# Kernel tuning notes

Hardware: AMD Instinct MI355X
Metric: run time of the kernel (lower is better)

Reference implementation:

```python
import jax, jax.numpy as jnp
import numpy as np

B, S, D = 4, 2048, 512
E, K = 8, 2
MH = 4 * D      # resmlp mlp hidden
EH = 2 * D      # expert hidden
EPS = 1e-5


def setup_inputs() -> dict:
    key = jax.random.key(0)
    ks = jax.random.split(key, 16)
    s = 0.02
    return {
        "x": jax.random.normal(ks[0], (B, S, D), dtype=jnp.float32),
        "ln1_g": jnp.ones((D,), jnp.float32), "ln1_b": jnp.zeros((D,), jnp.float32),
        "w1": jax.random.normal(ks[1], (D, MH), jnp.float32) * s,
        "b1": jnp.zeros((MH,), jnp.float32),
        "w2": jax.random.normal(ks[2], (MH, D), jnp.float32) * s,
        "b2": jnp.zeros((D,), jnp.float32),
        "ln2_g": jnp.ones((D,), jnp.float32), "ln2_b": jnp.zeros((D,), jnp.float32),
        "wr": jax.random.normal(ks[3], (E, D), jnp.float32) * s,
        "ew1": jax.random.normal(ks[4], (E, D, EH), jnp.float32) * s,
        "eb1": jnp.zeros((E, EH), jnp.float32),
        "ew2": jax.random.normal(ks[5], (E, EH, D), jnp.float32) * s,
        "eb2": jnp.zeros((E, D), jnp.float32),
        "lnf_g": jnp.ones((D,), jnp.float32), "lnf_b": jnp.zeros((D,), jnp.float32),
    }


def _ln(z, g, b):
    m = z.mean(-1, keepdims=True)
    v = ((z - m) ** 2).mean(-1, keepdims=True)
    return (z - m) * jax.lax.rsqrt(v + EPS) * g + b


def reference(x, ln1_g, ln1_b, w1, b1, w2, b2, ln2_g, ln2_b,
              wr, ew1, eb1, ew2, eb2, lnf_g, lnf_b):
    # ---- ResidualMLPBlock (eval mode: dropout is identity) ----
    h = _ln(x, ln1_g, ln1_b)
    h = jax.nn.gelu(h @ w1 + b1, approximate=False) @ w2 + b2
    x = x + h
    x = _ln(x, ln2_g, ln2_b) + x
    # ---- MoE (eval: no jitter noise, aux_loss = 0) ----
    xf = x.reshape(-1, D)              # [N, D], N = B*S
    n = xf.shape[0]
    probs = jax.nn.softmax(xf @ wr.T, axis=-1)          # [N, E]
    topv, topi = jax.lax.top_k(probs, K)                # [N, K]
    topv = topv / topv.sum(-1, keepdims=True)
    # dense per-token gate per expert: sum over k of renormalized prob where idx==j
    gates = jnp.zeros((n, E), xf.dtype).at[jnp.arange(n)[:, None], topi].add(topv)
    # per-expert MLP over all tokens (masked scatter-combine via gates)
    he = jax.nn.gelu(jnp.einsum("nd,edh->enh", xf, ew1) + eb1[:, None, :],
                     approximate=False)                 # [E, N, 2D]
    ye = jnp.einsum("enh,ehd->end", he, ew2) + eb2[:, None, :]  # [E, N, D]
    out = jnp.einsum("ne,end->nd", gates, ye).reshape(B, S, D)
    # ---- final LayerNorm ----
    out = _ln(out, lnf_g, lnf_b)
    aux_loss = jnp.zeros((), x.dtype)  # eval mode
    return out, aux_loss
```

## Files before the change

### kernel.cpp

```cpp
#include <hip/hip_runtime.h>

#define NTOK 8192
#define DIM  512
#define MHID 2048
#define EHID 1024
#define NEXP 8
#define RBLK 64

using half_t = _Float16;
typedef _Float16 f16x8 __attribute__((ext_vector_type(8)));
typedef float    f32x16 __attribute__((ext_vector_type(16)));

#define MFMA32(a, b, c) __builtin_amdgcn_mfma_f32_32x32x16_f16((a), (b), (c), 0, 0, 0)

typedef const __attribute__((address_space(1))) void* gas_ptr;
typedef __attribute__((address_space(3))) void*       las_ptr;
__device__ __forceinline__ void gl16(const void* g, void* l) {
    __builtin_amdgcn_global_load_lds((gas_ptr)g, (las_ptr)l, 16, 0, 0);
}

__device__ __forceinline__ float gelu_exact(float v) {
    return 0.5f * v * (1.0f + erff(v * 0.70710678118654752f));
}

__device__ __forceinline__ float block_sum4(float v, float* red, int tid) {
#pragma unroll
    for (int off = 32; off; off >>= 1) v += __shfl_down(v, off);
    if ((tid & 63) == 0) red[tid >> 6] = v;
    __syncthreads();
    float r = red[0] + red[1] + red[2] + red[3];
    __syncthreads();
    return r;
}

__global__ __launch_bounds__(256) void ln1_split_kernel(
    const float* __restrict__ x, const float* __restrict__ g, const float* __restrict__ b,
    half_t* __restrict__ xh, half_t* __restrict__ xl)
{
    const int row = blockIdx.x, tid = threadIdx.x;
    __shared__ float red[4];
    const size_t base = (size_t)row * DIM;
    float2 v = reinterpret_cast<const float2*>(x + base)[tid];
    float mean = block_sum4(v.x + v.y, red, tid) * (1.0f / DIM);
    float d0 = v.x - mean, d1 = v.y - mean;
    float var = block_sum4(d0 * d0 + d1 * d1, red, tid) * (1.0f / DIM);
    float rstd = rsqrtf(var + 1e-5f);
    int d = tid * 2;
    float y0 = d0 * rstd * g[d]     + b[d];
    float y1 = d1 * rstd * g[d + 1] + b[d + 1];
    half_t h0 = (half_t)y0, h1 = (half_t)y1;
    xh[base + d] = h0;  xh[base + d + 1] = h1;
    xl[base + d]     = (half_t)(y0 - (float)h0);
    xl[base + d + 1] = (half_t)(y1 - (float)h1);
}

__global__ __launch_bounds__(256) void resid_ln2_kernel(
    const float* __restrict__ x, float* __restrict__ p0, const float* __restrict__ p1,
    const float* __restrict__ b2,
    const float* __restrict__ g, const float* __restrict__ b,
    half_t* __restrict__ x3h)
{
    const int row = blockIdx.x, tid = threadIdx.x;
    __shared__ float red[4];
    const size_t base = (size_t)row * DIM;
    float2 xv = reinterpret_cast<const float2*>(x + base)[tid];
    float2 h0 = reinterpret_cast<float2*>(p0 + base)[tid];
    float2 h1 = reinterpret_cast<const float2*>(p1 + base)[tid];
    float2 bb = reinterpret_cast<const float2*>(b2)[tid];
    float z0 = xv.x + h0.x + h1.x + bb.x, z1 = xv.y + h0.y + h1.y + bb.y;
    float mean = block_sum4(z0 + z1, red, tid) * (1.0f / DIM);
    float d0 = z0 - mean, d1 = z1 - mean;
    float var = block_sum4(d0 * d0 + d1 * d1, red, tid) * (1.0f / DIM);
    float rstd = rsqrtf(var + 1e-5f);
    int d = tid * 2;
    float y0 = d0 * rstd * g[d]     + b[d]     + z0;
    float y1 = d1 * rstd * g[d + 1] + b[d + 1] + z1;
    float2 o; o.x = y0; o.y = y1;
    reinterpret_cast<float2*>(p0 + base)[tid] = o;
    x3h[base + d]     = (half_t)y0;
    x3h[base + d + 1] = (half_t)y1;
}

__global__ void transpose_split_kernel(const float* __restrict__ in,
                                       half_t* __restrict__ oh, half_t* __restrict__ ol,
                                       int R, int C)
{
    __shared__ float t[32][33];
    const size_t mo = (size_t)blockIdx.z * (size_t)R * (size_t)C;
    const int c0 = blockIdx.x * 32, r0 = blockIdx.y * 32;
    const int tx = threadIdx.x, ty = threadIdx.y;
    for (int i = ty; i < 32; i += 8) t[i][tx] = in[mo + (size_t)(r0 + i) * C + c0 + tx];
    __syncthreads();
    for (int i = ty; i < 32; i += 8) {
        float v = t[tx][i];
        size_t o = mo + (size_t)(c0 + i) * R + r0 + tx;
        half_t h = (half_t)v;
        oh[o] = h;
        if (ol) ol[o] = (half_t)(v - (float)h);
    }
}

template <int EPI>
__global__ __launch_bounds__(256) void gemm3_kernel(
    const half_t* __restrict__ A0, const half_t* __restrict__ A1,
    const half_t* __restrict__ B0, const half_t* __restrict__ B1,
    const float* __restrict__ bias,
    float* __restrict__ Cf0, float* __restrict__ Cf1,
    half_t* __restrict__ Ch, half_t* __restrict__ Cl,
    int Nc, int K, int Ktile)
{
    __shared__ __align__(16) half_t As0[128 * 32];
    __shared__ __align__(16) half_t As1[128 * 32];
    __shared__ __align__(16) half_t Bs0[128 * 32];
    __shared__ __align__(16) half_t Bs1[128 * 32];
    const int m0 = blockIdx.x * 128, n0 = blockIdx.y * 128;
    const int kbeg = blockIdx.z * Ktile;
    float* Cf = blockIdx.z ? Cf1 : Cf0;
    const int tid = threadIdx.x;
    const int lane = tid & 63, wid = tid >> 6;
    const int wr = wid >> 1, wc = wid & 1;

    const int c0 = tid, c1 = tid + 256;
    const int r0 = c0 >> 2, s0 = (c0 & 3) ^ ((r0 >> 1) & 3);
    const int r1 = c1 >> 2, s1 = (c1 & 3) ^ ((r1 >> 1) & 3);
    const size_t aoff0 = (size_t)(m0 + r0) * K + kbeg + s0 * 8;
    const size_t aoff1 = (size_t)(m0 + r1) * K + kbeg + s1 * 8;
    const size_t boff0 = (size_t)(n0 + r0) * K + kbeg + s0 * 8;
    const size_t boff1 = (size_t)(n0 + r1) * K + kbeg + s1 * 8;

    const int l31 = lane & 31, l5 = lane >> 5;
    int oa[2][2], ob[2][2];
#pragma unroll
    for (int i = 0; i < 2; i++)
#pragma unroll
        for (int kh = 0; kh < 2; kh++) {
            int ra = wr * 64 + i * 32 + l31;
            oa[i][kh] = ra * 32 + (((l5 + kh * 2) ^ ((ra >> 1) & 3)) << 3);
            int rb = wc * 64 + i * 32 + l31;
            ob[i][kh] = rb * 32 + (((l5 + kh * 2) ^ ((rb >> 1) & 3)) << 3);
        }

    f32x16 acc[2][2];
#pragma unroll
    for (int i = 0; i < 2; i++)
#pragma unroll
        for (int j = 0; j < 2; j++)
#pragma unroll
            for (int q = 0; q < 16; q++) acc[i][j][q] = 0.f;

#pragma unroll 1
    for (int k0 = 0; k0 < Ktile; k0 += 32) {
        __syncthreads();
        gl16(A0 + aoff0 + k0, As0 + c0 * 8);
        gl16(A0 + aoff1 + k0, As0 + c1 * 8);
        gl16(A1 + aoff0 + k0, As1 + c0 * 8);
        gl16(A1 + aoff1 + k0, As1 + c1 * 8);
        gl16(B0 + boff0 + k0, Bs0 + c0 * 8);
        gl16(B0 + boff1 + k0, Bs0 + c1 * 8);
        gl16(B1 + boff0 + k0, Bs1 + c0 * 8);
        gl16(B1 + boff1 + k0, Bs1 + c1 * 8);
        __syncthreads();
#pragma unroll
        for (int kh = 0; kh < 2; kh++) {
            f16x8 ah0 = *(const f16x8*)(As0 + oa[0][kh]);
            f16x8 ah1 = *(const f16x8*)(As0 + oa[1][kh]);
            f16x8 al0 = *(const f16x8*)(As1 + oa[0][kh]);
            f16x8 al1 = *(const f16x8*)(As1 + oa[1][kh]);
            f16x8 bh0 = *(const f16x8*)(Bs0 + ob[0][kh]);
            f16x8 bh1 = *(const f16x8*)(Bs0 + ob[1][kh]);
            f16x8 bl0 = *(const f16x8*)(Bs1 + ob[0][kh]);
            f16x8 bl1 = *(const f16x8*)(Bs1 + ob[1][kh]);
            acc[0][0] = MFMA32(ah0, bh0, acc[0][0]);
            acc[0][0] = MFMA32(al0, bh0, acc[0][0]);
            acc[0][0] = MFMA32(ah0, bl0, acc[0][0]);
            acc[0][1] = MFMA32(ah0, bh1, acc[0][1]);
            acc[0][1] = MFMA32(al0, bh1, acc[0][1]);
            acc[0][1] = MFMA32(ah0, bl1, acc[0][1]);
            acc[1][0] = MFMA32(ah1, bh0, acc[1][0]);
            acc[1][0] = MFMA32(al1, bh0, acc[1][0]);
            acc[1][0] = MFMA32(ah1, bl0, acc[1][0]);
            acc[1][1] = MFMA32(ah1, bh1, acc[1][1]);
            acc[1][1] = MFMA32(al1, bh1, acc[1][1]);
            acc[1][1] = MFMA32(ah1, bl1, acc[1][1]);
        }
    }

    const int er = 4 * l5;
#pragma unroll
    for (int i = 0; i < 2; i++)
#pragma unroll
        for (int j = 0; j < 2; j++) {
            int cc = n0 + wc * 64 + j * 32 + l31;
            float bv = (EPI == 1) ? bias[cc] : 0.f;
#pragma unroll
            for (int reg = 0; reg < 16; reg++) {
                int rr = m0 + wr * 64 + i * 32 + er + 8 * (reg >> 2) + (reg & 3);
                float v = acc[i][j][reg] + bv;
                size_t o = (size_t)rr * Nc + cc;
                if (EPI == 1) {
                    float ge = gelu_exact(v);
                    half_t h = (half_t)ge;
                    Ch[o] = h;
                    Cl[o] = (half_t)(ge - (float)h);
                } else {
                    Cf[o] = v;
                }
            }
        }
}

__global__ __launch_bounds__(256) void router_kernel(
    const float* __restrict__ x3, const float* __restrict__ wrm,
    int* __restrict__ cnt, int* __restrict__ aid, float* __restrict__ gate)
{
    __shared__ float wl[NEXP][DIM];
    __shared__ int   texp[RBLK * 2];
    __shared__ float tgate[RBLK * 2];
    __shared__ int   lslot[RBLK * 2];
    __shared__ int   lcnt[NEXP], lbase[NEXP];
    const int tid = threadIdx.x;
    for (int i = tid; i < NEXP * DIM / 4; i += 256)
        reinterpret_cast<float4*>(&wl[0][0])[i] = reinterpret_cast<const float4*>(wrm)[i];
    if (tid < NEXP) lcnt[tid] = 0;
    __syncthreads();
    const int w = tid >> 6, lane = tid & 63;
#pragma unroll 1
    for (int t = 0; t < RBLK / 4; ++t) {
        const int lt = w * (RBLK / 4) + t;
        const int token = blockIdx.x * RBLK + lt;
        const float* xr = x3 + (size_t)token * DIM;
        float a[NEXP];
#pragma unroll
        for (int e = 0; e < NEXP; e++) a[e] = 0.f;
#pragma unroll
        for (int d0 = 0; d0 < DIM; d0 += 64) {
            float xv = xr[d0 + lane];
#pragma unroll
            for (int e = 0; e < NEXP; e++) a[e] += xv * wl[e][d0 + lane];
        }
#pragma unroll
        for (int e = 0; e < NEXP; e++)
#pragma unroll
            for (int off = 32; off; off >>= 1) a[e] += __shfl_xor(a[e], off);
        if (lane == 0) {
            int i1 = 0; float v1 = a[0];
#pragma unroll
            for (int e = 1; e < NEXP; e++) if (a[e] > v1) { v1 = a[e]; i1 = e; }
            int i2 = -1; float v2 = -3.4e38f;
#pragma unroll
            for (int e = 0; e < NEXP; e++) if (e != i1 && a[e] > v2) { v2 = a[e]; i2 = e; }
            float e2 = expf(v2 - v1);
            float g1 = 1.0f / (1.0f + e2);
            texp[lt * 2]      = i1; tgate[lt * 2]      = g1;
            texp[lt * 2 + 1]  = i2; tgate[lt * 2 + 1]  = 1.0f - g1;
        }
    }
    __syncthreads();
    if (tid < RBLK * 2) lslot[tid] = atomicAdd(&lcnt[texp[tid]], 1);
    __syncthreads();
    if (tid < NEXP) lbase[tid] = atomicAdd(&cnt[tid * 32], lcnt[tid]);
    __syncthreads();
    if (tid < RBLK * 2) {
        const int e = texp[tid];
        const int asg = blockIdx.x * (RBLK * 2) + tid;
        aid[e * NTOK + lbase[e] + lslot[tid]] = asg;
        gate[asg] = tgate[tid];
    }
}

__global__ __launch_bounds__(256) void egemm1_kernel(
    const half_t* __restrict__ X,
    const half_t* __restrict__ W,
    const float* __restrict__ eb1,
    const int* __restrict__ cnt, const int* __restrict__ aid,
    half_t* __restrict__ He)
{
    const int bid = blockIdx.x;
    const int e = bid >> 9, rem = bid & 511;
    const int mt = rem >> 3, nt = rem & 7;
    const int ne = cnt[e * 32];
    if (mt * 128 >= ne) return;
    __shared__ __align__(16) half_t As[128 * 32];
    __shared__ __align__(16) half_t Bs[128 * 32];
    __shared__ int rowmap[128];
    const int tid = threadIdx.x;
    if (tid < 128) {
        int slot = mt * 128 + tid;
        rowmap[tid] = (slot < ne) ? aid[e * NTOK + slot] : -1;
    }
    __syncthreads();
    const int lane = tid & 63, wid = tid >> 6;
    const int wr = wid >> 1, wc = wid & 1;
    const int c0 = tid, c1 = tid + 256;
    const int r0 = c0 >> 2, s0 = (c0 & 3) ^ ((r0 >> 1) & 3);
    const int r1 = c1 >> 2, s1 = (c1 & 3) ^ ((r1 >> 1) & 3);
    const int a0r = rowmap[r0], a1r = rowmap[r1];
    const half_t* pa0 = X + (size_t)(a0r >= 0 ? (a0r >> 1) : 0) * DIM + s0 * 8;
    const half_t* pa1 = X + (size_t)(a1r >= 0 ? (a1r >> 1) : 0) * DIM + s1 * 8;
    const half_t* pb0 = W + (size_t)e * EHID * DIM + (size_t)(nt * 128 + r0) * DIM + s0 * 8;
    const half_t* pb1 = W + (size_t)e * EHID * DIM + (size_t)(nt * 128 + r1) * DIM + s1 * 8;

    const int l31 = lane & 31, l5 = lane >> 5;
    int oa[2][2], ob[2][2];
#pragma unroll
    for (int i = 0; i < 2; i++)
#pragma unroll
        for (int kh = 0; kh < 2; kh++) {
            int ra = wr * 64 + i * 32 + l31;
            oa[i][kh] = ra * 32 + (((l5 + kh * 2) ^ ((ra >> 1) & 3)) << 3);
            int rb = wc * 64 + i * 32 + l31;
            ob[i][kh] = rb * 32 + (((l5 + kh * 2) ^ ((rb >> 1) & 3)) << 3);
        }
    f32x16 acc[2][2];
#pragma unroll
    for (int i = 0; i < 2; i++)
#pragma unroll
        for (int j = 0; j < 2; j++)
#pragma unroll
            for (int q = 0; q < 16; q++) acc[i][j][q] = 0.f;

#pragma unroll 1
    for (int k0 = 0; k0 < DIM; k0 += 32) {
        __syncthreads();
        gl16(pa0 + k0, As + c0 * 8);
        gl16(pa1 + k0, As + c1 * 8);
        gl16(pb0 + k0, Bs + c0 * 8);
        gl16(pb1 + k0, Bs + c1 * 8);
        __syncthreads();
#pragma unroll
        for (int kh = 0; kh < 2; kh++) {
            f16x8 a0 = *(const f16x8*)(As + oa[0][kh]);
            f16x8 a1 = *(const f16x8*)(As + oa[1][kh]);
            f16x8 b0 = *(const f16x8*)(Bs + ob[0][kh]);
            f16x8 b1 = *(const f16x8*)(Bs + ob[1][kh]);
            acc[0][0] = MFMA32(a0, b0, acc[0][0]);
            acc[0][1] = MFMA32(a0, b1, acc[0][1]);
            acc[1][0] = MFMA32(a1, b0, acc[1][0]);
            acc[1][1] = MFMA32(a1, b1, acc[1][1]);
        }
    }
    const int er = 4 * l5;
#pragma unroll
    for (int i = 0; i < 2; i++)
#pragma unroll
        for (int reg = 0; reg < 16; reg++) {
            int rloc = wr * 64 + i * 32 + er + 8 * (reg >> 2) + (reg & 3);
            int a = rowmap[rloc];
            if (a >= 0) {
#pragma unroll
                for (int j = 0; j < 2; j++) {
                    int cc = nt * 128 + wc * 64 + j * 32 + l31;
                    float v = acc[i][j][reg] + eb1[e * EHID + cc];
                    He[(size_t)a * EHID + cc] = (half_t)gelu_exact(v);
                }
            }
        }
}

__global__ __launch_bounds__(256) void egemm2_kernel(
    const half_t* __restrict__ Hin,
    const half_t* __restrict__ W,
    const float* __restrict__ eb2,
    const int* __restrict__ cnt, const int* __restrict__ aid,
    const float* __restrict__ gate,
    float* __restrict__ Ye)
{
    const int bid = blockIdx.x;
    const int e = bid >> 8, rem = bid & 255;
    const int mt = rem >> 2, nt = rem & 3;
    const int ne = cnt[e * 32];
    if (mt * 128 >= ne) return;
    __shared__ __align__(16) half_t As[128 * 32];
    __shared__ __align__(16) half_t Bs[128 * 32];
    __shared__ int rowmap[128];
    const int tid = threadIdx.x;
    if (tid < 128) {
        int slot = mt * 128 + tid;
        rowmap[tid] = (slot < ne) ? aid[e * NTOK + slot] : -1;
    }
    __syncthreads();
    const int lane = tid & 63, wid = tid >> 6;
    const int wr = wid >> 1, wc = wid & 1;
    const int c0 = tid, c1 = tid + 256;
    const int r0 = c0 >> 2, s0 = (c0 & 3) ^ ((r0 >> 1) & 3);
    const int r1 = c1 >> 2, s1 = (c1 & 3) ^ ((r1 >> 1) & 3);
    const int a0r = rowmap[r0], a1r = rowmap[r1];
    const half_t* pa0 = Hin + (size_t)(a0r >= 0 ? a0r : 0) * EHID + s0 * 8;
    const half_t* pa1 = Hin + (size_t)(a1r >= 0 ? a1r : 0) * EHID + s1 * 8;
    const half_t* pb0 = W + (size_t)e * DIM * EHID + (size_t)(nt * 128 + r0) * EHID + s0 * 8;
    const half_t* pb1 = W + (size_t)e * DIM * EHID + (size_t)(nt * 128 + r1) * EHID + s1 * 8;

    const int l31 = lane & 31, l5 = lane >> 5;
    int oa[2][2], ob[2][2];
#pragma unroll
    for (int i = 0; i < 2; i++)
#pragma unroll
        for (int kh = 0; kh < 2; kh++) {
            int ra = wr * 64 + i * 32 + l31;
            oa[i][kh] = ra * 32 + (((l5 + kh * 2) ^ ((ra >> 1) & 3)) << 3);
            int rb = wc * 64 + i * 32 + l31;
            ob[i][kh] = rb * 32 + (((l5 + kh * 2) ^ ((rb >> 1) & 3)) << 3);
        }
    f32x16 acc[2][2];
#pragma unroll
    for (int i = 0; i < 2; i++)
#pragma unroll
        for (int j = 0; j < 2; j++)
#pragma unroll
            for (int q = 0; q < 16; q++) acc[i][j][q] = 0.f;

#pragma unroll 1
    for (int k0 = 0; k0 < EHID; k0 += 32) {
        __syncthreads();
        gl16(pa0 + k0, As + c0 * 8);
        gl16(pa1 + k0, As + c1 * 8);
        gl16(pb0 + k0, Bs + c0 * 8);
        gl16(pb1 + k0, Bs + c1 * 8);
        __syncthreads();
#pragma unroll
        for (int kh = 0; kh < 2; kh++) {
            f16x8 a0 = *(const f16x8*)(As + oa[0][kh]);
            f16x8 a1 = *(const f16x8*)(As + oa[1][kh]);
            f16x8 b0 = *(const f16x8*)(Bs + ob[0][kh]);
            f16x8 b1 = *(const f16x8*)(Bs + ob[1][kh]);
            acc[0][0] = MFMA32(a0, b0, acc[0][0]);
            acc[0][1] = MFMA32(a0, b1, acc[0][1]);
            acc[1][0] = MFMA32(a1, b0, acc[1][0]);
            acc[1][1] = MFMA32(a1, b1, acc[1][1]);
        }
    }
    const int er = 4 * l5;
#pragma unroll
    for (int i = 0; i < 2; i++)
#pragma unroll
        for (int reg = 0; reg < 16; reg++) {
            int rloc = wr * 64 + i * 32 + er + 8 * (reg >> 2) + (reg & 3);
            int a = rowmap[rloc];
            if (a >= 0) {
                float gv = gate[a];
#pragma unroll
                for (int j = 0; j < 2; j++) {
                    int cc = nt * 128 + wc * 64 + j * 32 + l31;
                    float v = (acc[i][j][reg] + eb2[e * DIM + cc]) * gv;
                    Ye[(size_t)a * DIM + cc] = v;
                }
            }
        }
}

__global__ __launch_bounds__(256) void combine_lnf_kernel(
    const float* __restrict__ Ye, const float* __restrict__ g, const float* __restrict__ b,
    float* __restrict__ out)
{
    const int t = blockIdx.x, tid = threadIdx.x;
    __shared__ float red[4];
    float2 y0 = reinterpret_cast<const float2*>(Ye + (size_t)(2 * t) * DIM)[tid];
    float2 y1 = reinterpret_cast<const float2*>(Ye + (size_t)(2 * t + 1) * DIM)[tid];
    float z0 = y0.x + y1.x, z1 = y0.y + y1.y;
    float mean = block_sum4(z0 + z1, red, tid) * (1.0f / DIM);
    float d0 = z0 - mean, d1 = z1 - mean;
    float var = block_sum4(d0 * d0 + d1 * d1, red, tid) * (1.0f / DIM);
    float rstd = rsqrtf(var + 1e-5f);
    int d = tid * 2;
    out[(size_t)t * DIM + d]     = d0 * rstd * g[d]     + b[d];
    out[(size_t)t * DIM + d + 1] = d1 * rstd * g[d + 1] + b[d + 1];
    if (t == 0 && tid == 0) out[(size_t)NTOK * DIM] = 0.f;
}

__global__ void zero_cnt_kernel(int* cnt) {
    cnt[threadIdx.x] = 0;
}

extern "C" void kernel_launch(void* const* d_in, const int* in_sizes, int n_in,
                              void* d_out, int out_size, void* d_ws, size_t ws_size,
                              hipStream_t stream)
{
    (void)in_sizes; (void)n_in; (void)out_size; (void)ws_size;
    const float* x    = (const float*)d_in[0];
    const float* ln1g = (const float*)d_in[1];
    const float* ln1b = (const float*)d_in[2];
    const float* w1   = (const float*)d_in[3];
    const float* b1   = (const float*)d_in[4];
    const float* w2   = (const float*)d_in[5];
    const float* b2   = (const float*)d_in[6];
    const float* ln2g = (const float*)d_in[7];
    const float* ln2b = (const float*)d_in[8];
    const float* wrm  = (const float*)d_in[9];
    const float* ew1  = (const float*)d_in[10];
    const float* eb1  = (const float*)d_in[11];
    const float* ew2  = (const float*)d_in[12];
    const float* eb2  = (const float*)d_in[13];
    const float* lnfg = (const float*)d_in[14];
    const float* lnfb = (const float*)d_in[15];
    float* out = (float*)d_out;

    char* w = (char*)d_ws;
    size_t off = 0;
    auto take = [&](size_t bytes) {
        char* p = w + off;
        off += bytes;
        off = (off + 255) & ~(size_t)255;
        return p;
    };
    half_t* xh_h  = (half_t*)take((size_t)NTOK * DIM * 2);
    half_t* xh_l  = (half_t*)take((size_t)NTOK * DIM * 2);
    half_t* w1t_h = (half_t*)take((size_t)DIM * MHID * 2);
    half_t* w1t_l = (half_t*)take((size_t)DIM * MHID * 2);
    half_t* w2t_h = (half_t*)take((size_t)MHID * DIM * 2);
    half_t* w2t_l = (half_t*)take((size_t)MHID * DIM * 2);
    char*   big   = take((size_t)NTOK * MHID * 2 * 2);
    half_t* a1h   = (half_t*)big;
    half_t* a1l   = (half_t*)(big + (size_t)NTOK * MHID * 2);
    half_t* heh   = (half_t*)big;
    float*  yef   = (float*)(big + (size_t)NTOK * MHID * 2);
    float*  x3f   = (float*)take((size_t)NTOK * DIM * 4);
    half_t* x3h   = (half_t*)take((size_t)NTOK * DIM * 2);
    half_t* ew1t  = (half_t*)take((size_t)NEXP * DIM * EHID * 2);
    half_t* ew2t  = (half_t*)take((size_t)NEXP * EHID * DIM * 2);
    int*    cnt   = (int*)take(1024);
    int*    aid   = (int*)take((size_t)NEXP * NTOK * 4);
    float*  gate  = (float*)take((size_t)NTOK * 2 * 4);

    float* p0 = x3f;
    float* p1 = (float*)xh_h;

    zero_cnt_kernel<<<1, 256, 0, stream>>>(cnt);
    ln1_split_kernel<<<NTOK, 256, 0, stream>>>(x, ln1g, ln1b, xh_h, xh_l);
    transpose_split_kernel<<<dim3(MHID / 32, DIM / 32, 1), dim3(32, 8), 0, stream>>>(w1, w1t_h, w1t_l, DIM, MHID);
    transpose_split_kernel<<<dim3(DIM / 32, MHID / 32, 1), dim3(32, 8), 0, stream>>>(w2, w2t_h, w2t_l, MHID, DIM);
    transpose_split_kernel<<<dim3(EHID / 32, DIM / 32, NEXP), dim3(32, 8), 0, stream>>>(ew1, ew1t, (half_t*)0, DIM, EHID);
    transpose_split_kernel<<<dim3(DIM / 32, EHID / 32, NEXP), dim3(32, 8), 0, stream>>>(ew2, ew2t, (half_t*)0, EHID, DIM);
    gemm3_kernel<1><<<dim3(NTOK / 128, MHID / 128, 1), 256, 0, stream>>>(
        xh_h, xh_l, w1t_h, w1t_l, b1, (float*)0, (float*)0, a1h, a1l, MHID, DIM, DIM);
    gemm3_kernel<0><<<dim3(NTOK / 128, DIM / 128, 2), 256, 0, stream>>>(
        a1h, a1l, w2t_h, w2t_l, (const float*)0, p0, p1, (half_t*)0, (half_t*)0, DIM, MHID, MHID / 2);
    resid_ln2_kernel<<<NTOK, 256, 0, stream>>>(x, p0, p1, b2, ln2g, ln2b, x3h);
    router_kernel<<<NTOK / RBLK, 256, 0, stream>>>(x3f, wrm, cnt, aid, gate);
    egemm1_kernel<<<NEXP * (NTOK / 128) * (EHID / 128), 256, 0, stream>>>(x3h, ew1t, eb1, cnt, aid, heh);
    egemm2_kernel<<<NEXP * (NTOK / 128) * (DIM / 128), 256, 0, stream>>>(heh, ew2t, eb2, cnt, aid, gate, yef);
    combine_lnf_kernel<<<NTOK, 256, 0, stream>>>(yef, lnfg, lnfb, out);
}
```

Baseline: 324.4 us.

## Double-buffer LDS tiles in dense and expert GEMM kernels

Converts the shared-memory A/B tiles of gemm3, egemm1 and egemm2 to two buffers each. The next K-slice is now issued with global_load_lds before computing on the current one, so the MFMA work can overlap the global-to-LDS traffic instead of stalling at every slice. This doubles LDS use per block (64KB for the split-f16 gemm3), which may lower occupancy. The loop steps two slices at a time and assumes the K extent is a multiple of 64.

```diff
diff --git a/kernel.cpp b/kernel.cpp
--- a/kernel.cpp
+++ b/kernel.cpp
@@ -109,10 +109,10 @@
     half_t* __restrict__ Ch, half_t* __restrict__ Cl,
     int Nc, int K, int Ktile)
 {
-    __shared__ __align__(16) half_t As0[128 * 32];
-    __shared__ __align__(16) half_t As1[128 * 32];
-    __shared__ __align__(16) half_t Bs0[128 * 32];
-    __shared__ __align__(16) half_t Bs1[128 * 32];
+    __shared__ __align__(16) half_t As0[2][128 * 32];
+    __shared__ __align__(16) half_t As1[2][128 * 32];
+    __shared__ __align__(16) half_t Bs0[2][128 * 32];
+    __shared__ __align__(16) half_t Bs1[2][128 * 32];
     const int m0 = blockIdx.x * 128, n0 = blockIdx.y * 128;
     const int kbeg = blockIdx.z * Ktile;
     float* Cf = blockIdx.z ? Cf1 : Cf0;
@@ -148,28 +148,27 @@
 #pragma unroll
             for (int q = 0; q < 16; q++) acc[i][j][q] = 0.f;
 
-#pragma unroll 1
-    for (int k0 = 0; k0 < Ktile; k0 += 32) {
-        __syncthreads();
-        gl16(A0 + aoff0 + k0, As0 + c0 * 8);
-        gl16(A0 + aoff1 + k0, As0 + c1 * 8);
-        gl16(A1 + aoff0 + k0, As1 + c0 * 8);
-        gl16(A1 + aoff1 + k0, As1 + c1 * 8);
-        gl16(B0 + boff0 + k0, Bs0 + c0 * 8);
-        gl16(B0 + boff1 + k0, Bs0 + c1 * 8);
-        gl16(B1 + boff0 + k0, Bs1 + c0 * 8);
-        gl16(B1 + boff1 + k0, Bs1 + c1 * 8);
-        __syncthreads();
+    auto stage = [&](int bsel, int k0) {
+        gl16(A0 + aoff0 + k0, &As0[bsel][c0 * 8]);
+        gl16(A0 + aoff1 + k0, &As0[bsel][c1 * 8]);
+        gl16(A1 + aoff0 + k0, &As1[bsel][c0 * 8]);
+        gl16(A1 + aoff1 + k0, &As1[bsel][c1 * 8]);
+        gl16(B0 + boff0 + k0, &Bs0[bsel][c0 * 8]);
+        gl16(B0 + boff1 + k0, &Bs0[bsel][c1 * 8]);
+        gl16(B1 + boff0 + k0, &Bs1[bsel][c0 * 8]);
+        gl16(B1 + boff1 + k0, &Bs1[bsel][c1 * 8]);
+    };
+    auto compute = [&](int bsel) {
 #pragma unroll
         for (int kh = 0; kh < 2; kh++) {
-            f16x8 ah0 = *(const f16x8*)(As0 + oa[0][kh]);
-            f16x8 ah1 = *(const f16x8*)(As0 + oa[1][kh]);
-            f16x8 al0 = *(const f16x8*)(As1 + oa[0][kh]);
-            f16x8 al1 = *(const f16x8*)(As1 + oa[1][kh]);
-            f16x8 bh0 = *(const f16x8*)(Bs0 + ob[0][kh]);
-            f16x8 bh1 = *(const f16x8*)(Bs0 + ob[1][kh]);
-            f16x8 bl0 = *(const f16x8*)(Bs1 + ob[0][kh]);
-            f16x8 bl1 = *(const f16x8*)(Bs1 + ob[1][kh]);
+            f16x8 ah0 = *(const f16x8*)(&As0[bsel][0] + oa[0][kh]);
+            f16x8 ah1 = *(const f16x8*)(&As0[bsel][0] + oa[1][kh]);
+            f16x8 al0 = *(const f16x8*)(&As1[bsel][0] + oa[0][kh]);
+            f16x8 al1 = *(const f16x8*)(&As1[bsel][0] + oa[1][kh]);
+            f16x8 bh0 = *(const f16x8*)(&Bs0[bsel][0] + ob[0][kh]);
+            f16x8 bh1 = *(const f16x8*)(&Bs0[bsel][0] + ob[1][kh]);
+            f16x8 bl0 = *(const f16x8*)(&Bs1[bsel][0] + ob[0][kh]);
+            f16x8 bl1 = *(const f16x8*)(&Bs1[bsel][0] + ob[1][kh]);
             acc[0][0] = MFMA32(ah0, bh0, acc[0][0]);
             acc[0][0] = MFMA32(al0, bh0, acc[0][0]);
             acc[0][0] = MFMA32(ah0, bl0, acc[0][0]);
@@ -183,6 +182,17 @@
             acc[1][1] = MFMA32(al1, bh1, acc[1][1]);
             acc[1][1] = MFMA32(ah1, bl1, acc[1][1]);
         }
+    };
+
+    stage(0, 0);
+#pragma unroll 1
+    for (int k0 = 0; k0 < Ktile; k0 += 64) {
+        __syncthreads();
+        if (k0 + 32 < Ktile) stage(1, k0 + 32);
+        compute(0);
+        __syncthreads();
+        if (k0 + 64 < Ktile) stage(0, k0 + 64);
+        compute(1);
     }
 
     const int er = 4 * l5;
@@ -280,8 +290,8 @@
     const int mt = rem >> 3, nt = rem & 7;
     const int ne = cnt[e * 32];
     if (mt * 128 >= ne) return;
-    __shared__ __align__(16) half_t As[128 * 32];
-    __shared__ __align__(16) half_t Bs[128 * 32];
+    __shared__ __align__(16) half_t As[2][128 * 32];
+    __shared__ __align__(16) half_t Bs[2][128 * 32];
     __shared__ int rowmap[128];
     const int tid = threadIdx.x;
     if (tid < 128) {
@@ -319,25 +329,35 @@
 #pragma unroll
             for (int q = 0; q < 16; q++) acc[i][j][q] = 0.f;
 
-#pragma unroll 1
-    for (int k0 = 0; k0 < DIM; k0 += 32) {
-        __syncthreads();
-        gl16(pa0 + k0, As + c0 * 8);
-        gl16(pa1 + k0, As + c1 * 8);
-        gl16(pb0 + k0, Bs + c0 * 8);
-        gl16(pb1 + k0, Bs + c1 * 8);
-        __syncthreads();
+    auto stage = [&](int bsel, int k0) {
+        gl16(pa0 + k0, &As[bsel][c0 * 8]);
+        gl16(pa1 + k0, &As[bsel][c1 * 8]);
+        gl16(pb0 + k0, &Bs[bsel][c0 * 8]);
+        gl16(pb1 + k0, &Bs[bsel][c1 * 8]);
+    };
+    auto compute = [&](int bsel) {
 #pragma unroll
         for (int kh = 0; kh < 2; kh++) {
-            f16x8 a0 = *(const f16x8*)(As + oa[0][kh]);
-            f16x8 a1 = *(const f16x8*)(As + oa[1][kh]);
-            f16x8 b0 = *(const f16x8*)(Bs + ob[0][kh]);
-            f16x8 b1 = *(const f16x8*)(Bs + ob[1][kh]);
+            f16x8 a0 = *(const f16x8*)(&As[bsel][0] + oa[0][kh]);
+            f16x8 a1 = *(const f16x8*)(&As[bsel][0] + oa[1][kh]);
+            f16x8 b0 = *(const f16x8*)(&Bs[bsel][0] + ob[0][kh]);
+            f16x8 b1 = *(const f16x8*)(&Bs[bsel][0] + ob[1][kh]);
             acc[0][0] = MFMA32(a0, b0, acc[0][0]);
             acc[0][1] = MFMA32(a0, b1, acc[0][1]);
             acc[1][0] = MFMA32(a1, b0, acc[1][0]);
             acc[1][1] = MFMA32(a1, b1, acc[1][1]);
         }
+    };
+
+    stage(0, 0);
+#pragma unroll 1
+    for (int k0 = 0; k0 < DIM; k0 += 64) {
+        __syncthreads();
+        if (k0 + 32 < DIM) stage(1, k0 + 32);
+        compute(0);
+        __syncthreads();
+        if (k0 + 64 < DIM) stage(0, k0 + 64);
+        compute(1);
     }
     const int er = 4 * l5;
 #pragma unroll
@@ -370,8 +390,8 @@
     const int mt = rem >> 2, nt = rem & 3;
     const int ne = cnt[e * 32];
     if (mt * 128 >= ne) return;
-    __shared__ __align__(16) half_t As[128 * 32];
-    __shared__ __align__(16) half_t Bs[128 * 32];
+    __shared__ __align__(16) half_t As[2][128 * 32];
+    __shared__ __align__(16) half_t Bs[2][128 * 32];
     __shared__ int rowmap[128];
     const int tid = threadIdx.x;
     if (tid < 128) {
@@ -409,25 +429,35 @@
 #pragma unroll
             for (int q = 0; q < 16; q++) acc[i][j][q] = 0.f;
 
-#pragma unroll 1
-    for (int k0 = 0; k0 < EHID; k0 += 32) {
-        __syncthreads();
-        gl16(pa0 + k0, As + c0 * 8);
-        gl16(pa1 + k0, As + c1 * 8);
-        gl16(pb0 + k0, Bs + c0 * 8);
-        gl16(pb1 + k0, Bs + c1 * 8);
-        __syncthreads();
+    auto stage = [&](int bsel, int k0) {
+        gl16(pa0 + k0, &As[bsel][c0 * 8]);
+        gl16(pa1 + k0, &As[bsel][c1 * 8]);
+        gl16(pb0 + k0, &Bs[bsel][c0 * 8]);
+        gl16(pb1 + k0, &Bs[bsel][c1 * 8]);
+    };
+    auto compute = [&](int bsel) {
 #pragma unroll
         for (int kh = 0; kh < 2; kh++) {
-            f16x8 a0 = *(const f16x8*)(As + oa[0][kh]);
-            f16x8 a1 = *(const f16x8*)(As + oa[1][kh]);
-            f16x8 b0 = *(const f16x8*)(Bs + ob[0][kh]);
-            f16x8 b1 = *(const f16x8*)(Bs + ob[1][kh]);
+            f16x8 a0 = *(const f16x8*)(&As[bsel][0] + oa[0][kh]);
+            f16x8 a1 = *(const f16x8*)(&As[bsel][0] + oa[1][kh]);
+            f16x8 b0 = *(const f16x8*)(&Bs[bsel][0] + ob[0][kh]);
+            f16x8 b1 = *(const f16x8*)(&Bs[bsel][0] + ob[1][kh]);
             acc[0][0] = MFMA32(a0, b0, acc[0][0]);
             acc[0][1] = MFMA32(a0, b1, acc[0][1]);
             acc[1][0] = MFMA32(a1, b0, acc[1][0]);
             acc[1][1] = MFMA32(a1, b1, acc[1][1]);
         }
+    };
+
+    stage(0, 0);
+#pragma unroll 1
+    for (int k0 = 0; k0 < EHID; k0 += 64) {
+        __syncthreads();
+        if (k0 + 32 < EHID) stage(1, k0 + 32);
+        compute(0);
+        __syncthreads();
+        if (k0 + 64 < EHID) stage(0, k0 + 64);
+        compute(1);
     }
     const int er = 4 * l5;
 #pragma unroll
```

After: 326.9 us. Within noise of the previous version (+0.8%).
